# Kernel tuning notes

Measured on AMD Instinct MI355X. Metric: run time of the kernel, lower is better.

## Reference

```python
import jax, jax.numpy as jnp
import numpy as np

INPUT_DIM = 512


def setup_inputs() -> dict:
    key = jax.random.key(0)
    ks = jax.random.split(key, 9)
    B = 262144
    d = INPUT_DIM
    inp = {
        "combined": jax.random.normal(ks[0], (B, 2 * d), dtype=jnp.float32),
        "W_in": jax.random.normal(ks[1], (d, 128), dtype=jnp.float32) / np.sqrt(d),
        "b_in": jax.random.normal(ks[2], (128,), dtype=jnp.float32) * 0.01,
        "W1": jax.random.normal(ks[3], (128, 128), dtype=jnp.float32) / np.sqrt(128.0),
        "b1": jax.random.normal(ks[4], (128,), dtype=jnp.float32) * 0.01,
        "W2": jax.random.normal(ks[5], (128, 64), dtype=jnp.float32) / np.sqrt(128.0),
        "b2": jax.random.normal(ks[6], (64,), dtype=jnp.float32) * 0.01,
        "W_out": jax.random.normal(ks[7], (128, 1), dtype=jnp.float32) / np.sqrt(128.0),
        "b_out": jax.random.normal(ks[8], (1,), dtype=jnp.float32) * 0.01,
    }
    return inp


def reference(combined, W_in, b_in, W1, b1, W2, b2, W_out, b_out):
    d = INPUT_DIM
    # Build per-sample 2-node graphs: nodes = (subj, obj). Shape [B, 2, d]
    x = jnp.stack([combined[:, :d], combined[:, d:]], axis=1)
    h = jax.nn.relu(x @ W_in + b_in)  # [B, 2, 128]

    # GCNConv on the 2-node graph (edges 0<->1 + default self-loops):
    # deg(i)=2, edge norm = 1/sqrt(2)*1/sqrt(2)=0.5, so both nodes get
    # 0.5*(h0 W + h1 W) + b == mean over nodes, transformed.
    def gcn(h, W, b):
        m = jnp.mean(h, axis=1, keepdims=True) @ W + b  # [B, 1, out]
        return jnp.broadcast_to(m, (h.shape[0], 2, W.shape[1]))

    h = jax.nn.relu(gcn(h, W1, b1))  # [B, 2, 128]
    h = jax.nn.relu(gcn(h, W2, b2))  # [B, 2, 64]

    combined_nodes = jnp.concatenate([h[:, 0], h[:, 1]], axis=-1)  # [B, 128]
    score = combined_nodes @ W_out + b_out  # [B, 1]
    return jax.nn.sigmoid(score)
```

## Files before the change

kernel.cpp:

```cpp
#include <hip/hip_runtime.h>
#include <hip/hip_bf16.h>
#include <cstdint>
#include <cstddef>


#define NROWS   524288
#define NSAMP   262144

typedef __attribute__((ext_vector_type(8))) short  bf16x8;
typedef __attribute__((ext_vector_type(4))) float  f32x4;

__device__ __forceinline__ unsigned short f2bf(float f) {
    unsigned u = __float_as_uint(f);
    u += 0x7fffu + ((u >> 16) & 1u);
    return (unsigned short)(u >> 16);
}

__device__ __forceinline__ bf16x8 cvt8(f32x4 lo, f32x4 hi) {
    bf16x8 r;
    r[0] = (short)f2bf(lo[0]); r[1] = (short)f2bf(lo[1]);
    r[2] = (short)f2bf(lo[2]); r[3] = (short)f2bf(lo[3]);
    r[4] = (short)f2bf(hi[0]); r[5] = (short)f2bf(hi[1]);
    r[6] = (short)f2bf(hi[2]); r[7] = (short)f2bf(hi[3]);
    return r;
}

#define WS_M     0
#define WS_WIN   67108864
#define WS_W1    67239936
#define WS_W2    67272704
#define WS_WEFF  67289088

__global__ void prep_kernel(const float* __restrict__ W_in,
                            const float* __restrict__ W1,
                            const float* __restrict__ W2,
                            const float* __restrict__ W_out,
                            unsigned short* __restrict__ fWin,
                            unsigned short* __restrict__ fW1,
                            unsigned short* __restrict__ fW2,
                            float* __restrict__ weff) {
    int tid = blockIdx.x * 256 + threadIdx.x;
    if (tid < 65536) {
        int e = tid;
        int j = e & 7, l = (e >> 3) & 63, rest = e >> 9;
        int n = rest & 7, kt = rest >> 3;
        int lg = l >> 4;
        int kin = (j < 4) ? (lg * 4 + j) : (16 + lg * 4 + (j - 4));
        int k = kt * 32 + kin;
        int col = n * 16 + (l & 15);
        fWin[e] = f2bf(W_in[k * 128 + col]);
    } else if (tid < 65536 + 16384) {
        int e = tid - 65536;
        int j = e & 7, l = (e >> 3) & 63, rest = e >> 9;
        int n = rest & 7, kt = rest >> 3;
        int k = kt * 32 + ((l >> 4) << 3) + j;
        int col = n * 16 + (l & 15);
        fW1[e] = f2bf(W1[k * 128 + col]);
    } else if (tid < 65536 + 16384 + 8192) {
        int e = tid - 65536 - 16384;
        int j = e & 7, l = (e >> 3) & 63, rest = e >> 9;
        int n = rest & 3, kt = rest >> 2;
        int k = kt * 32 + ((l >> 4) << 3) + j;
        int col = n * 16 + (l & 15);
        fW2[e] = f2bf(W2[k * 64 + col]);
    } else if (tid < 65536 + 16384 + 8192 + 64) {
        int c = tid - (65536 + 16384 + 8192);
        weff[c] = W_out[c] + W_out[64 + c];
    }
}

__global__ void __launch_bounds__(512) __attribute__((amdgpu_waves_per_eu(2, 2)))
kA(const float* __restrict__ A,
   const unsigned short* __restrict__ fWin,
   const float* __restrict__ b_in,
   unsigned short* __restrict__ M) {
    __shared__ unsigned short lwin[65536];
    __shared__ unsigned short bounce[8][1088];
    {
        const f32x4* src = (const f32x4*)fWin;
        f32x4* dst = (f32x4*)lwin;
        int tid = threadIdx.x;
        #pragma unroll
        for (int i = 0; i < 16; ++i) dst[i * 512 + tid] = src[i * 512 + tid];
    }
    __syncthreads();
    const int w = threadIdx.x >> 6, l = threadIdx.x & 63;
    const int lr = l & 15, lg = l >> 4;
    float binv[8];
    #pragma unroll
    for (int n = 0; n < 8; ++n) binv[n] = b_in[n * 16 + lr];
    unsigned short* bw = &bounce[w][0];

    for (int t = blockIdx.x; t < NROWS / 256; t += 256) {
        const size_t rowbase = (size_t)t * 256 + (size_t)w * 32;
        const float* a0 = A + (rowbase + lr) * 512 + lg * 4;
        const float* a1 = a0 + (size_t)16 * 512;

        f32x4 acc[2][8];
        #pragma unroll
        for (int rt = 0; rt < 2; ++rt)
            #pragma unroll
            for (int n = 0; n < 8; ++n) acc[rt][n] = (f32x4){0.f, 0.f, 0.f, 0.f};

        f32x4 st[3][2][2][2];
        #pragma unroll
        for (int pc = 0; pc < 2; ++pc) {
            #pragma unroll
            for (int ks = 0; ks < 2; ++ks) {
                st[pc][0][ks][0] = *(const f32x4*)(a0 + pc * 64 + ks * 32);
                st[pc][0][ks][1] = *(const f32x4*)(a0 + pc * 64 + ks * 32 + 16);
                st[pc][1][ks][0] = *(const f32x4*)(a1 + pc * 64 + ks * 32);
                st[pc][1][ks][1] = *(const f32x4*)(a1 + pc * 64 + ks * 32 + 16);
            }
        }
        #pragma unroll
        for (int c = 0; c < 8; ++c) {
            const int cb = c % 3;
            if (c < 6) {
                const int nb = (c + 2) % 3;
                #pragma unroll
                for (int ks = 0; ks < 2; ++ks) {
                    st[nb][0][ks][0] = *(const f32x4*)(a0 + (c + 2) * 64 + ks * 32);
                    st[nb][0][ks][1] = *(const f32x4*)(a0 + (c + 2) * 64 + ks * 32 + 16);
                    st[nb][1][ks][0] = *(const f32x4*)(a1 + (c + 2) * 64 + ks * 32);
                    st[nb][1][ks][1] = *(const f32x4*)(a1 + (c + 2) * 64 + ks * 32 + 16);
                }
            }
            #pragma unroll
            for (int ks = 0; ks < 2; ++ks) {
                const int kg = c * 2 + ks;
                bf16x8 af0 = cvt8(st[cb][0][ks][0], st[cb][0][ks][1]);
                bf16x8 af1 = cvt8(st[cb][1][ks][0], st[cb][1][ks][1]);
                #pragma unroll
                for (int n = 0; n < 8; ++n) {
                    bf16x8 bf = *(const bf16x8*)&lwin[((kg * 8 + n) * 64 + l) * 8];
                    acc[0][n] = __builtin_amdgcn_mfma_f32_16x16x32_bf16(af0, bf, acc[0][n], 0, 0, 0);
                    acc[1][n] = __builtin_amdgcn_mfma_f32_16x16x32_bf16(af1, bf, acc[1][n], 0, 0, 0);
                }
            }
        }
        #pragma unroll
        for (int rt = 0; rt < 2; ++rt) {
            #pragma unroll
            for (int n = 0; n < 8; ++n) {
                const float b = binv[n];
                float h0 = fmaxf(acc[rt][n][0] + b, 0.f);
                float h1 = fmaxf(acc[rt][n][1] + b, 0.f);
                float h2 = fmaxf(acc[rt][n][2] + b, 0.f);
                float h3 = fmaxf(acc[rt][n][3] + b, 0.f);
                bw[(2 * lg) * 136 + n * 16 + lr]     = f2bf(0.5f * (h0 + h1));
                bw[(2 * lg + 1) * 136 + n * 16 + lr] = f2bf(0.5f * (h2 + h3));
            }
            asm volatile("s_waitcnt lgkmcnt(0)" ::: "memory");
            const size_t sampbase = (rowbase >> 1) + rt * 8;
            #pragma unroll
            for (int r = 0; r < 2; ++r) {
                int ci = r * 64 + l;
                int s = ci >> 4, cc = ci & 15;
                bf16x8 v = *(const bf16x8*)&bw[s * 136 + cc * 8];
                *(bf16x8*)&M[(sampbase + s) * 128 + cc * 8] = v;
            }
        }
    }
}

__global__ void __launch_bounds__(256, 2)
kB(const unsigned short* __restrict__ M,
   const unsigned short* __restrict__ fW1,
   const unsigned short* __restrict__ fW2,
   const float* __restrict__ weff,
   const float* __restrict__ b1,
   const float* __restrict__ b2,
   const float* __restrict__ b_out,
   float* __restrict__ out) {
    __shared__ unsigned short lw1[16384];
    __shared__ unsigned short lw2[8192];
    __shared__ unsigned short bounce[4][2048];
    {
        int tid = threadIdx.x;
        const f32x4* s1 = (const f32x4*)fW1;
        f32x4* d1 = (f32x4*)lw1;
        #pragma unroll
        for (int i = 0; i < 8; ++i) d1[i * 256 + tid] = s1[i * 256 + tid];
        const f32x4* s2 = (const f32x4*)fW2;
        f32x4* d2 = (f32x4*)lw2;
        #pragma unroll
        for (int i = 0; i < 4; ++i) d2[i * 256 + tid] = s2[i * 256 + tid];
    }
    __syncthreads();
    const int w = threadIdx.x >> 6, l = threadIdx.x & 63;
    const int lr = l & 15, lg = l >> 4;
    float b1v[8], b2v[4], wev[4];
    #pragma unroll
    for (int n = 0; n < 8; ++n) b1v[n] = b1[n * 16 + lr];
    #pragma unroll
    for (int n = 0; n < 4; ++n) { b2v[n] = b2[n * 16 + lr]; wev[n] = weff[n * 16 + lr]; }
    const float bo = b_out[0];

    for (int t = blockIdx.x; t < NSAMP / 64; t += 512) {
        const int s0 = t * 64 + w * 16;
        f32x4 acc1[8];
        #pragma unroll
        for (int n = 0; n < 8; ++n) acc1[n] = (f32x4){0.f, 0.f, 0.f, 0.f};
        const unsigned short* arow = M + (size_t)(s0 + lr) * 128 + lg * 8;
        #pragma unroll
        for (int ks = 0; ks < 4; ++ks) {
            bf16x8 af = *(const bf16x8*)(arow + ks * 32);
            #pragma unroll
            for (int n = 0; n < 8; ++n) {
                bf16x8 bf = *(const bf16x8*)&lw1[((ks * 8 + n) * 64 + l) * 8];
                acc1[n] = __builtin_amdgcn_mfma_f32_16x16x32_bf16(af, bf, acc1[n], 0, 0, 0);
            }
        }
        #pragma unroll
        for (int n = 0; n < 8; ++n) {
            #pragma unroll
            for (int r = 0; r < 4; ++r) {
                float g = fmaxf(acc1[n][r] + b1v[n], 0.f);
                int row = lg * 4 + r, col = n * 16 + lr;
                int boff = row * 256 + ((col * 2) ^ ((row & 7) << 4));
                bounce[w][boff >> 1] = f2bf(g);
            }
        }
        f32x4 acc2[4];
        #pragma unroll
        for (int n = 0; n < 4; ++n) acc2[n] = (f32x4){0.f, 0.f, 0.f, 0.f};
        #pragma unroll
        for (int ks = 0; ks < 4; ++ks) {
            int roff = lr * 256 + ((ks * 64 + lg * 16) ^ ((lr & 7) << 4));
            bf16x8 af2 = *(const bf16x8*)((const char*)&bounce[w][0] + roff);
            #pragma unroll
            for (int n = 0; n < 4; ++n) {
                bf16x8 bf = *(const bf16x8*)&lw2[((ks * 4 + n) * 64 + l) * 8];
                acc2[n] = __builtin_amdgcn_mfma_f32_16x16x32_bf16(af2, bf, acc2[n], 0, 0, 0);
            }
        }
        float p0 = 0.f, p1 = 0.f, p2 = 0.f, p3 = 0.f;
        #pragma unroll
        for (int n = 0; n < 4; ++n) {
            p0 += fmaxf(acc2[n][0] + b2v[n], 0.f) * wev[n];
            p1 += fmaxf(acc2[n][1] + b2v[n], 0.f) * wev[n];
            p2 += fmaxf(acc2[n][2] + b2v[n], 0.f) * wev[n];
            p3 += fmaxf(acc2[n][3] + b2v[n], 0.f) * wev[n];
        }
        #pragma unroll
        for (int m = 1; m < 16; m <<= 1) {
            p0 += __shfl_xor(p0, m);
            p1 += __shfl_xor(p1, m);
            p2 += __shfl_xor(p2, m);
            p3 += __shfl_xor(p3, m);
        }
        float s0f = 1.f / (1.f + expf(-(p0 + bo)));
        float s1f = 1.f / (1.f + expf(-(p1 + bo)));
        float s2f = 1.f / (1.f + expf(-(p2 + bo)));
        float s3f = 1.f / (1.f + expf(-(p3 + bo)));
        if (lr < 4) {
            float v = (lr == 0) ? s0f : (lr == 1) ? s1f : (lr == 2) ? s2f : s3f;
            out[s0 + lg * 4 + lr] = v;
        }
    }
}

extern "C" void kernel_launch(void* const* d_in, const int* in_sizes, int n_in,
                              void* d_out, int out_size, void* d_ws, size_t ws_size,
                              hipStream_t stream) {
    const float* combined = (const float*)d_in[0];
    const float* W_in  = (const float*)d_in[1];
    const float* b_in  = (const float*)d_in[2];
    const float* W1    = (const float*)d_in[3];
    const float* b1    = (const float*)d_in[4];
    const float* W2    = (const float*)d_in[5];
    const float* b2    = (const float*)d_in[6];
    const float* W_out = (const float*)d_in[7];
    const float* b_out = (const float*)d_in[8];
    float* out = (float*)d_out;

    char* ws = (char*)d_ws;
    unsigned short* M    = (unsigned short*)(ws + WS_M);
    unsigned short* fWin = (unsigned short*)(ws + WS_WIN);
    unsigned short* fW1  = (unsigned short*)(ws + WS_W1);
    unsigned short* fW2  = (unsigned short*)(ws + WS_W2);
    float* weff          = (float*)(ws + WS_WEFF);

    prep_kernel<<<(65536 + 16384 + 8192 + 64 + 255) / 256, 256, 0, stream>>>(
        W_in, W1, W2, W_out, fWin, fW1, fW2, weff);
    kA<<<256, 512, 0, stream>>>(combined, fWin, b_in, M);
    kB<<<512, 256, 0, stream>>>(M, fW1, fW2, weff, b1, b2, b_out, out);
}
```

Before: 279.4 us.

## Fuse GCN MLP stages into input-projection kernel, dropping intermediate buffer

Merges the second kernel into the first, so the per-sample mean embedding goes through the W1 and W2 layers straight from LDS and the sigmoid output is written directly. This removes the 64MB bf16 intermediate write and read plus one kernel launch. The A-tile prefetch now uses a 4-deep ring that runs on into the next tile across loop iterations, and the bf16 conversion uses the packed v_cvt_pk_bf16_f32 instruction. In exchange, the W1 and W2 fragments are read from global memory (through cache) rather than LDS, and register pressure goes up.

```diff
diff --git a/kernel.cpp b/kernel.cpp
--- a/kernel.cpp
+++ b/kernel.cpp
@@ -17,19 +17,18 @@
 }
 
 __device__ __forceinline__ bf16x8 cvt8(f32x4 lo, f32x4 hi) {
-    bf16x8 r;
-    r[0] = (short)f2bf(lo[0]); r[1] = (short)f2bf(lo[1]);
-    r[2] = (short)f2bf(lo[2]); r[3] = (short)f2bf(lo[3]);
-    r[4] = (short)f2bf(hi[0]); r[5] = (short)f2bf(hi[1]);
-    r[6] = (short)f2bf(hi[2]); r[7] = (short)f2bf(hi[3]);
-    return r;
-}
-
-#define WS_M     0
-#define WS_WIN   67108864
-#define WS_W1    67239936
-#define WS_W2    67272704
-#define WS_WEFF  67289088
+    union { unsigned u[4]; bf16x8 v; } r;
+    asm("v_cvt_pk_bf16_f32 %0, %1, %2" : "=v"(r.u[0]) : "v"(lo[0]), "v"(lo[1]));
+    asm("v_cvt_pk_bf16_f32 %0, %1, %2" : "=v"(r.u[1]) : "v"(lo[2]), "v"(lo[3]));
+    asm("v_cvt_pk_bf16_f32 %0, %1, %2" : "=v"(r.u[2]) : "v"(hi[0]), "v"(hi[1]));
+    asm("v_cvt_pk_bf16_f32 %0, %1, %2" : "=v"(r.u[3]) : "v"(hi[2]), "v"(hi[3]));
+    return r.v;
+}
+
+#define WS_WIN   0
+#define WS_W1    131072
+#define WS_W2    163840
+#define WS_WEFF  180224
 
 __global__ void prep_kernel(const float* __restrict__ W_in,
                             const float* __restrict__ W1,
@@ -72,13 +71,19 @@
 __global__ void __launch_bounds__(512) __attribute__((amdgpu_waves_per_eu(2, 2)))
 kA(const float* __restrict__ A,
    const unsigned short* __restrict__ fWin,
+   const unsigned short* __restrict__ fW1,
+   const unsigned short* __restrict__ fW2,
+   const float* __restrict__ weff,
    const float* __restrict__ b_in,
-   unsigned short* __restrict__ M) {
-    __shared__ unsigned short lwin[65536];
-    __shared__ unsigned short bounce[8][1088];
+   const float* __restrict__ b1,
+   const float* __restrict__ b2,
+   const float* __restrict__ b_out,
+   float* __restrict__ out) {
+    __shared__ __align__(16) unsigned short lds[81920];
+    unsigned short* lwin = lds;
     {
         const f32x4* src = (const f32x4*)fWin;
-        f32x4* dst = (f32x4*)lwin;
+        f32x4* dst = (f32x4*)lds;
         int tid = threadIdx.x;
         #pragma unroll
         for (int i = 0; i < 16; ++i) dst[i * 512 + tid] = src[i * 512 + tid];
@@ -86,44 +91,51 @@
     __syncthreads();
     const int w = threadIdx.x >> 6, l = threadIdx.x & 63;
     const int lr = l & 15, lg = l >> 4;
-    float binv[8];
+    unsigned short* bw = lds + 65536 + w * 2048;
+    float binv[8], b1v[8], b2v[4], wev[4];
     #pragma unroll
-    for (int n = 0; n < 8; ++n) binv[n] = b_in[n * 16 + lr];
-    unsigned short* bw = &bounce[w][0];
-
-    for (int t = blockIdx.x; t < NROWS / 256; t += 256) {
-        const size_t rowbase = (size_t)t * 256 + (size_t)w * 32;
-        const float* a0 = A + (rowbase + lr) * 512 + lg * 4;
-        const float* a1 = a0 + (size_t)16 * 512;
-
+    for (int n = 0; n < 8; ++n) { binv[n] = b_in[n * 16 + lr]; b1v[n] = b1[n * 16 + lr]; }
+    #pragma unroll
+    for (int n = 0; n < 4; ++n) { b2v[n] = b2[n * 16 + lr]; wev[n] = weff[n * 16 + lr]; }
+    const float bo = b_out[0];
+
+    const size_t TSTR = (size_t)65536 * 512;
+    const float* a0 = A + ((size_t)blockIdx.x * 256 + (size_t)w * 32 + lr) * 512 + lg * 4;
+    const float* a1 = a0 + (size_t)16 * 512;
+
+    f32x4 st[4][2][2][2];
+    #pragma unroll
+    for (int pc = 0; pc < 2; ++pc) {
+        #pragma unroll
+        for (int ks = 0; ks < 2; ++ks) {
+            st[pc][0][ks][0] = *(const f32x4*)(a0 + pc * 64 + ks * 32);
+            st[pc][0][ks][1] = *(const f32x4*)(a0 + pc * 64 + ks * 32 + 16);
+            st[pc][1][ks][0] = *(const f32x4*)(a1 + pc * 64 + ks * 32);
+            st[pc][1][ks][1] = *(const f32x4*)(a1 + pc * 64 + ks * 32 + 16);
+        }
+    }
+
+    for (int i = 0; i < 8; ++i) {
+        const size_t nextoff = (i == 7) ? 0 : TSTR;
         f32x4 acc[2][8];
         #pragma unroll
         for (int rt = 0; rt < 2; ++rt)
             #pragma unroll
             for (int n = 0; n < 8; ++n) acc[rt][n] = (f32x4){0.f, 0.f, 0.f, 0.f};
 
-        f32x4 st[3][2][2][2];
-        #pragma unroll
-        for (int pc = 0; pc < 2; ++pc) {
-            #pragma unroll
-            for (int ks = 0; ks < 2; ++ks) {
-                st[pc][0][ks][0] = *(const f32x4*)(a0 + pc * 64 + ks * 32);
-                st[pc][0][ks][1] = *(const f32x4*)(a0 + pc * 64 + ks * 32 + 16);
-                st[pc][1][ks][0] = *(const f32x4*)(a1 + pc * 64 + ks * 32);
-                st[pc][1][ks][1] = *(const f32x4*)(a1 + pc * 64 + ks * 32 + 16);
-            }
-        }
         #pragma unroll
         for (int c = 0; c < 8; ++c) {
-            const int cb = c % 3;
-            if (c < 6) {
-                const int nb = (c + 2) % 3;
+            const int cb = c & 3;
+            {
+                const int nb = (c + 2) & 3;
+                const float* q0 = (c < 6) ? (a0 + (c + 2) * 64) : (a0 + nextoff + (c - 6) * 64);
+                const float* q1 = q0 + (size_t)16 * 512;
                 #pragma unroll
                 for (int ks = 0; ks < 2; ++ks) {
-                    st[nb][0][ks][0] = *(const f32x4*)(a0 + (c + 2) * 64 + ks * 32);
-                    st[nb][0][ks][1] = *(const f32x4*)(a0 + (c + 2) * 64 + ks * 32 + 16);
-                    st[nb][1][ks][0] = *(const f32x4*)(a1 + (c + 2) * 64 + ks * 32);
-                    st[nb][1][ks][1] = *(const f32x4*)(a1 + (c + 2) * 64 + ks * 32 + 16);
+                    st[nb][0][ks][0] = *(const f32x4*)(q0 + ks * 32);
+                    st[nb][0][ks][1] = *(const f32x4*)(q0 + ks * 32 + 16);
+                    st[nb][1][ks][0] = *(const f32x4*)(q1 + ks * 32);
+                    st[nb][1][ks][1] = *(const f32x4*)(q1 + ks * 32 + 16);
                 }
             }
             #pragma unroll
@@ -139,6 +151,7 @@
                 }
             }
         }
+
         #pragma unroll
         for (int rt = 0; rt < 2; ++rt) {
             #pragma unroll
@@ -148,68 +161,29 @@
                 float h1 = fmaxf(acc[rt][n][1] + b, 0.f);
                 float h2 = fmaxf(acc[rt][n][2] + b, 0.f);
                 float h3 = fmaxf(acc[rt][n][3] + b, 0.f);
-                bw[(2 * lg) * 136 + n * 16 + lr]     = f2bf(0.5f * (h0 + h1));
-                bw[(2 * lg + 1) * 136 + n * 16 + lr] = f2bf(0.5f * (h2 + h3));
-            }
-            asm volatile("s_waitcnt lgkmcnt(0)" ::: "memory");
-            const size_t sampbase = (rowbase >> 1) + rt * 8;
-            #pragma unroll
-            for (int r = 0; r < 2; ++r) {
-                int ci = r * 64 + l;
-                int s = ci >> 4, cc = ci & 15;
-                bf16x8 v = *(const bf16x8*)&bw[s * 136 + cc * 8];
-                *(bf16x8*)&M[(sampbase + s) * 128 + cc * 8] = v;
-            }
-        }
-    }
-}
-
-__global__ void __launch_bounds__(256, 2)
-kB(const unsigned short* __restrict__ M,
-   const unsigned short* __restrict__ fW1,
-   const unsigned short* __restrict__ fW2,
-   const float* __restrict__ weff,
-   const float* __restrict__ b1,
-   const float* __restrict__ b2,
-   const float* __restrict__ b_out,
-   float* __restrict__ out) {
-    __shared__ unsigned short lw1[16384];
-    __shared__ unsigned short lw2[8192];
-    __shared__ unsigned short bounce[4][2048];
-    {
-        int tid = threadIdx.x;
-        const f32x4* s1 = (const f32x4*)fW1;
-        f32x4* d1 = (f32x4*)lw1;
-        #pragma unroll
-        for (int i = 0; i < 8; ++i) d1[i * 256 + tid] = s1[i * 256 + tid];
-        const f32x4* s2 = (const f32x4*)fW2;
-        f32x4* d2 = (f32x4*)lw2;
-        #pragma unroll
-        for (int i = 0; i < 4; ++i) d2[i * 256 + tid] = s2[i * 256 + tid];
-    }
-    __syncthreads();
-    const int w = threadIdx.x >> 6, l = threadIdx.x & 63;
-    const int lr = l & 15, lg = l >> 4;
-    float b1v[8], b2v[4], wev[4];
-    #pragma unroll
-    for (int n = 0; n < 8; ++n) b1v[n] = b1[n * 16 + lr];
-    #pragma unroll
-    for (int n = 0; n < 4; ++n) { b2v[n] = b2[n * 16 + lr]; wev[n] = weff[n * 16 + lr]; }
-    const float bo = b_out[0];
-
-    for (int t = blockIdx.x; t < NSAMP / 64; t += 512) {
-        const int s0 = t * 64 + w * 16;
+                int row0 = rt * 8 + 2 * lg, row1 = row0 + 1;
+                int col2 = (n * 16 + lr) * 2;
+                *(unsigned short*)((char*)bw + row0 * 256 + (col2 ^ ((row0 & 7) << 4))) = f2bf(0.5f * (h0 + h1));
+                *(unsigned short*)((char*)bw + row1 * 256 + (col2 ^ ((row1 & 7) << 4))) = f2bf(0.5f * (h2 + h3));
+            }
+        }
+        asm volatile("s_waitcnt lgkmcnt(0)" ::: "memory");
+
+        bf16x8 a2[4];
+        #pragma unroll
+        for (int ks = 0; ks < 4; ++ks) {
+            int roff = lr * 256 + ((ks * 64 + lg * 16) ^ ((lr & 7) << 4));
+            a2[ks] = *(const bf16x8*)((const char*)bw + roff);
+        }
         f32x4 acc1[8];
         #pragma unroll
         for (int n = 0; n < 8; ++n) acc1[n] = (f32x4){0.f, 0.f, 0.f, 0.f};
-        const unsigned short* arow = M + (size_t)(s0 + lr) * 128 + lg * 8;
-        #pragma unroll
-        for (int ks = 0; ks < 4; ++ks) {
-            bf16x8 af = *(const bf16x8*)(arow + ks * 32);
+        #pragma unroll
+        for (int ks = 0; ks < 4; ++ks) {
             #pragma unroll
             for (int n = 0; n < 8; ++n) {
-                bf16x8 bf = *(const bf16x8*)&lw1[((ks * 8 + n) * 64 + l) * 8];
-                acc1[n] = __builtin_amdgcn_mfma_f32_16x16x32_bf16(af, bf, acc1[n], 0, 0, 0);
+                bf16x8 bfw = *(const bf16x8*)&fW1[(size_t)((ks * 8 + n) * 64 + l) * 8];
+                acc1[n] = __builtin_amdgcn_mfma_f32_16x16x32_bf16(a2[ks], bfw, acc1[n], 0, 0, 0);
             }
         }
         #pragma unroll
@@ -217,24 +191,31 @@
             #pragma unroll
             for (int r = 0; r < 4; ++r) {
                 float g = fmaxf(acc1[n][r] + b1v[n], 0.f);
-                int row = lg * 4 + r, col = n * 16 + lr;
-                int boff = row * 256 + ((col * 2) ^ ((row & 7) << 4));
-                bounce[w][boff >> 1] = f2bf(g);
-            }
+                int row = lg * 4 + r;
+                int col2 = (n * 16 + lr) * 2;
+                *(unsigned short*)((char*)bw + row * 256 + (col2 ^ ((row & 7) << 4))) = f2bf(g);
+            }
+        }
+        asm volatile("s_waitcnt lgkmcnt(0)" ::: "memory");
+
+        bf16x8 a3[4];
+        #pragma unroll
+        for (int ks = 0; ks < 4; ++ks) {
+            int roff = lr * 256 + ((ks * 64 + lg * 16) ^ ((lr & 7) << 4));
+            a3[ks] = *(const bf16x8*)((const char*)bw + roff);
         }
         f32x4 acc2[4];
         #pragma unroll
         for (int n = 0; n < 4; ++n) acc2[n] = (f32x4){0.f, 0.f, 0.f, 0.f};
         #pragma unroll
         for (int ks = 0; ks < 4; ++ks) {
-            int roff = lr * 256 + ((ks * 64 + lg * 16) ^ ((lr & 7) << 4));
-            bf16x8 af2 = *(const bf16x8*)((const char*)&bounce[w][0] + roff);
             #pragma unroll
             for (int n = 0; n < 4; ++n) {
-                bf16x8 bf = *(const bf16x8*)&lw2[((ks * 4 + n) * 64 + l) * 8];
-                acc2[n] = __builtin_amdgcn_mfma_f32_16x16x32_bf16(af2, bf, acc2[n], 0, 0, 0);
-            }
-        }
+                bf16x8 bfw = *(const bf16x8*)&fW2[(size_t)((ks * 4 + n) * 64 + l) * 8];
+                acc2[n] = __builtin_amdgcn_mfma_f32_16x16x32_bf16(a3[ks], bfw, acc2[n], 0, 0, 0);
+            }
+        }
+
         float p0 = 0.f, p1 = 0.f, p2 = 0.f, p3 = 0.f;
         #pragma unroll
         for (int n = 0; n < 4; ++n) {
@@ -250,6 +231,8 @@
             p2 += __shfl_xor(p2, m);
             p3 += __shfl_xor(p3, m);
         }
+        const size_t t = (size_t)blockIdx.x + (size_t)i * 256;
+        const size_t s0 = t * 128 + (size_t)w * 16;
         float s0f = 1.f / (1.f + expf(-(p0 + bo)));
         float s1f = 1.f / (1.f + expf(-(p1 + bo)));
         float s2f = 1.f / (1.f + expf(-(p2 + bo)));
@@ -258,6 +241,9 @@
             float v = (lr == 0) ? s0f : (lr == 1) ? s1f : (lr == 2) ? s2f : s3f;
             out[s0 + lg * 4 + lr] = v;
         }
+
+        a0 += nextoff;
+        a1 += nextoff;
     }
 }
 
@@ -276,7 +262,6 @@
     float* out = (float*)d_out;
 
     char* ws = (char*)d_ws;
-    unsigned short* M    = (unsigned short*)(ws + WS_M);
     unsigned short* fWin = (unsigned short*)(ws + WS_WIN);
     unsigned short* fW1  = (unsigned short*)(ws + WS_W1);
     unsigned short* fW2  = (unsigned short*)(ws + WS_W2);
@@ -284,6 +269,6 @@
 
     prep_kernel<<<(65536 + 16384 + 8192 + 64 + 255) / 256, 256, 0, stream>>>(
         W_in, W1, W2, W_out, fWin, fW1, fW2, weff);
-    kA<<<256, 512, 0, stream>>>(combined, fWin, b_in, M);
-    kB<<<512, 256, 0, stream>>>(M, fW1, fW2, weff, b1, b2, b_out, out);
-}
+    kA<<<256, 512, 0, stream>>>(combined, fWin, fW1, fW2, weff,
+                                b_in, b1, b2, b_out, out);
+}
```

Measured after the change: 393.1 us. 40.7% more time.

## Store intermediate in MFMA-fragment layout and use packed bf16 conversion

Applied to the files above, without the earlier changes.

kA now writes the per-sample mean activations into a fragment-ordered layout. It stages them through a swizzled per-wave LDS tile so that kB can load its MFMA A operands as contiguous 16-byte per-lane chunks, where before it used strided row reads. The float-to-bf16 conversion of inputs is replaced with the hardware v_cvt_pk_bf16_f32 instruction, which cuts VALU work in the main loop. The packed instruction's rounding may differ from the manual round-to-nearest-even on NaN edge cases, and the LDS bounce is enlarged.

```diff
diff --git a/kernel.cpp b/kernel.cpp
--- a/kernel.cpp
+++ b/kernel.cpp
@@ -10,6 +10,8 @@
 typedef __attribute__((ext_vector_type(8))) short  bf16x8;
 typedef __attribute__((ext_vector_type(4))) float  f32x4;
 
+#define LGKM0() asm volatile("s_waitcnt lgkmcnt(0)" ::: "memory")
+
 __device__ __forceinline__ unsigned short f2bf(float f) {
     unsigned u = __float_as_uint(f);
     u += 0x7fffu + ((u >> 16) & 1u);
@@ -17,12 +19,16 @@
 }
 
 __device__ __forceinline__ bf16x8 cvt8(f32x4 lo, f32x4 hi) {
-    bf16x8 r;
-    r[0] = (short)f2bf(lo[0]); r[1] = (short)f2bf(lo[1]);
-    r[2] = (short)f2bf(lo[2]); r[3] = (short)f2bf(lo[3]);
-    r[4] = (short)f2bf(hi[0]); r[5] = (short)f2bf(hi[1]);
-    r[6] = (short)f2bf(hi[2]); r[7] = (short)f2bf(hi[3]);
-    return r;
+    union { unsigned u[4]; bf16x8 v; } r;
+    asm("v_cvt_pk_bf16_f32 %0, %1, %2" : "=v"(r.u[0]) : "v"(lo[0]), "v"(lo[1]));
+    asm("v_cvt_pk_bf16_f32 %0, %1, %2" : "=v"(r.u[1]) : "v"(lo[2]), "v"(lo[3]));
+    asm("v_cvt_pk_bf16_f32 %0, %1, %2" : "=v"(r.u[2]) : "v"(hi[0]), "v"(hi[1]));
+    asm("v_cvt_pk_bf16_f32 %0, %1, %2" : "=v"(r.u[3]) : "v"(hi[2]), "v"(hi[3]));
+    return r.v;
+}
+
+__device__ __forceinline__ f32x4 mfma16(bf16x8 a, bf16x8 b, f32x4 c) {
+    return __builtin_amdgcn_mfma_f32_16x16x32_bf16(a, b, c, 0, 0, 0);
 }
 
 #define WS_M     0
@@ -73,12 +79,12 @@
 kA(const float* __restrict__ A,
    const unsigned short* __restrict__ fWin,
    const float* __restrict__ b_in,
-   unsigned short* __restrict__ M) {
-    __shared__ unsigned short lwin[65536];
-    __shared__ unsigned short bounce[8][1088];
+   unsigned short* __restrict__ Mf) {
+    __shared__ __align__(16) unsigned short lds[81920];
+    unsigned short* lwin = lds;
     {
         const f32x4* src = (const f32x4*)fWin;
-        f32x4* dst = (f32x4*)lwin;
+        f32x4* dst = (f32x4*)lds;
         int tid = threadIdx.x;
         #pragma unroll
         for (int i = 0; i < 16; ++i) dst[i * 512 + tid] = src[i * 512 + tid];
@@ -86,10 +92,10 @@
     __syncthreads();
     const int w = threadIdx.x >> 6, l = threadIdx.x & 63;
     const int lr = l & 15, lg = l >> 4;
+    char* bw = (char*)lds + 131072 + w * 4096;
     float binv[8];
     #pragma unroll
     for (int n = 0; n < 8; ++n) binv[n] = b_in[n * 16 + lr];
-    unsigned short* bw = &bounce[w][0];
 
     for (int t = blockIdx.x; t < NROWS / 256; t += 256) {
         const size_t rowbase = (size_t)t * 256 + (size_t)w * 32;
@@ -134,8 +140,8 @@
                 #pragma unroll
                 for (int n = 0; n < 8; ++n) {
                     bf16x8 bf = *(const bf16x8*)&lwin[((kg * 8 + n) * 64 + l) * 8];
-                    acc[0][n] = __builtin_amdgcn_mfma_f32_16x16x32_bf16(af0, bf, acc[0][n], 0, 0, 0);
-                    acc[1][n] = __builtin_amdgcn_mfma_f32_16x16x32_bf16(af1, bf, acc[1][n], 0, 0, 0);
+                    acc[0][n] = mfma16(af0, bf, acc[0][n]);
+                    acc[1][n] = mfma16(af1, bf, acc[1][n]);
                 }
             }
         }
@@ -148,24 +154,25 @@
                 float h1 = fmaxf(acc[rt][n][1] + b, 0.f);
                 float h2 = fmaxf(acc[rt][n][2] + b, 0.f);
                 float h3 = fmaxf(acc[rt][n][3] + b, 0.f);
-                bw[(2 * lg) * 136 + n * 16 + lr]     = f2bf(0.5f * (h0 + h1));
-                bw[(2 * lg + 1) * 136 + n * 16 + lr] = f2bf(0.5f * (h2 + h3));
-            }
-            asm volatile("s_waitcnt lgkmcnt(0)" ::: "memory");
-            const size_t sampbase = (rowbase >> 1) + rt * 8;
-            #pragma unroll
-            for (int r = 0; r < 2; ++r) {
-                int ci = r * 64 + l;
-                int s = ci >> 4, cc = ci & 15;
-                bf16x8 v = *(const bf16x8*)&bw[s * 136 + cc * 8];
-                *(bf16x8*)&M[(sampbase + s) * 128 + cc * 8] = v;
-            }
+                int s0i = rt * 8 + 2 * lg, s1i = s0i + 1;
+                int col2 = (n * 16 + lr) * 2;
+                *(unsigned short*)(bw + s0i * 256 + (col2 ^ ((s0i & 7) << 4))) = f2bf(0.5f * (h0 + h1));
+                *(unsigned short*)(bw + s1i * 256 + (col2 ^ ((s1i & 7) << 4))) = f2bf(0.5f * (h2 + h3));
+            }
+        }
+        LGKM0();
+        const size_t F = (size_t)t * 8 + (size_t)w;
+        #pragma unroll
+        for (int ks = 0; ks < 4; ++ks) {
+            int roff = lr * 256 + (((unsigned)(lg * 16 + ks * 64)) ^ ((lr & 7) << 4));
+            bf16x8 v = *(const bf16x8*)(bw + roff);
+            *(bf16x8*)&Mf[F * 2048 + ks * 512 + l * 8] = v;
         }
     }
 }
 
 __global__ void __launch_bounds__(256, 2)
-kB(const unsigned short* __restrict__ M,
+kB(const unsigned short* __restrict__ Mf,
    const unsigned short* __restrict__ fW1,
    const unsigned short* __restrict__ fW2,
    const float* __restrict__ weff,
@@ -199,13 +206,13 @@
 
     for (int t = blockIdx.x; t < NSAMP / 64; t += 512) {
         const int s0 = t * 64 + w * 16;
+        const size_t F = (size_t)t * 4 + (size_t)w;
         f32x4 acc1[8];
         #pragma unroll
         for (int n = 0; n < 8; ++n) acc1[n] = (f32x4){0.f, 0.f, 0.f, 0.f};
-        const unsigned short* arow = M + (size_t)(s0 + lr) * 128 + lg * 8;
         #pragma unroll
         for (int ks = 0; ks < 4; ++ks) {
-            bf16x8 af = *(const bf16x8*)(arow + ks * 32);
+            bf16x8 af = *(const bf16x8*)&Mf[F * 2048 + ks * 512 + l * 8];
             #pragma unroll
             for (int n = 0; n < 8; ++n) {
                 bf16x8 bf = *(const bf16x8*)&lw1[((ks * 8 + n) * 64 + l) * 8];
@@ -215,9 +222,9 @@
         #pragma unroll
         for (int n = 0; n < 8; ++n) {
             #pragma unroll
-            for (int r = 0; r < 4; ++r) {
-                float g = fmaxf(acc1[n][r] + b1v[n], 0.f);
-                int row = lg * 4 + r, col = n * 16 + lr;
+            for (int rr = 0; rr < 4; ++rr) {
+                float g = fmaxf(acc1[n][rr] + b1v[n], 0.f);
+                int row = lg * 4 + rr, col = n * 16 + lr;
                 int boff = row * 256 + ((col * 2) ^ ((row & 7) << 4));
                 bounce[w][boff >> 1] = f2bf(g);
             }
@@ -276,7 +283,7 @@
     float* out = (float*)d_out;
 
     char* ws = (char*)d_ws;
-    unsigned short* M    = (unsigned short*)(ws + WS_M);
+    unsigned short* Mf   = (unsigned short*)(ws + WS_M);
     unsigned short* fWin = (unsigned short*)(ws + WS_WIN);
     unsigned short* fW1  = (unsigned short*)(ws + WS_W1);
     unsigned short* fW2  = (unsigned short*)(ws + WS_W2);
@@ -284,6 +291,6 @@
 
     prep_kernel<<<(65536 + 16384 + 8192 + 64 + 255) / 256, 256, 0, stream>>>(
         W_in, W1, W2, W_out, fWin, fW1, fW2, weff);
-    kA<<<256, 512, 0, stream>>>(combined, fWin, b_in, M);
-    kB<<<512, 256, 0, stream>>>(M, fW1, fW2, weff, b1, b2, b_out, out);
-}
+    kA<<<256, 512, 0, stream>>>(combined, fWin, b_in, Mf);
+    kB<<<512, 256, 0, stream>>>(Mf, fW1, fW2, weff, b1, b2, b_out, out);
+}
```

After: 295.4 us. +5.7%, slower.
